# Kernel tuning notes

Hardware: AMD Instinct MI355X
Metric: run time of the kernel (lower is better)

Reference implementation:

```python
import jax, jax.numpy as jnp
import numpy as np

B, C, E, K = 16, 256, 9216, 4096  # meshes, channels, max input edges, target edges (out_channel)


def setup_inputs() -> dict:
    key = jax.random.key(0)
    k1, k2 = jax.random.split(key)
    x = jax.random.normal(k1, (B, C, E), dtype=jnp.float32)
    # ragged per-mesh edge counts, all >= K so pooling target is reachable
    edges_count = E - jax.random.randint(k2, (B,), 0, 512)
    return {"x": x, "edges_count": edges_count.astype(jnp.int64), "out_channel": K}


def reference(x, edges_count, out_channel):
    # Per-mesh edge saliency: squared sum over channels (torch.sum(x**2, dim=0)).
    score = jnp.sum(x * x, axis=1)  # [B, E]
    # Mask padded (invalid) edges beyond each mesh's edges_count so they are never kept.
    valid = jnp.arange(score.shape[-1]) < edges_count[:, None]
    score = jnp.where(valid, score, -jnp.inf)
    # Greedy collapse removes the lowest-score edges until out_channel edges remain:
    # keep the out_channel highest-score edges (descending sort + mask in the original).
    _, keep_idx = jax.lax.top_k(score, out_channel)  # [B, K]
    # Preserve original edge ordering of the surviving edges (mask-based rebuild).
    keep_idx = jnp.sort(keep_idx, axis=-1)
    # Gather surviving edge features -> [B, C, K]; matches view(B, -1, out_target).
    out = jnp.take_along_axis(x, keep_idx[:, None, :], axis=2)
    return out
```

## Files before the change

kernel.cpp:

```cpp
#include <hip/hip_runtime.h>
#include <hip/hip_bf16.h>

#define B_DIM 16
#define C_DIM 256
#define E_DIM 9216
#define K_DIM 4096
#define SEL_T 512
#define EPT   (E_DIM / SEL_T)

typedef float v4f __attribute__((ext_vector_type(4)));

__global__ __launch_bounds__(256) void score_kernel(
    const float* __restrict__ x, const void* __restrict__ ecp,
    unsigned* __restrict__ keys) {
  __shared__ double part[3][64];

  const int lane = threadIdx.x & 63;
  const int w = threadIdx.x >> 6;
  const int blk = blockIdx.x;
  const int b = blk / (E_DIM / 64);
  const int e = (blk % (E_DIM / 64)) * 64 + lane;

  const float* col =
      x + (size_t)b * C_DIM * E_DIM + (size_t)(w * 64) * E_DIM + e;

  double a0 = 0.0, a1 = 0.0;
#pragma unroll 8
  for (int c = 0; c < 64; c += 2) {
    float v0 = col[(size_t)(c + 0) * E_DIM];
    float v1 = col[(size_t)(c + 1) * E_DIM];
    a0 += (double)v0 * v0;
    a1 += (double)v1 * v1;
  }
  double s = a0 + a1;

  if (w) part[w - 1][lane] = s;
  __syncthreads();

  if (w == 0) {
    s += part[0][lane] + (part[1][lane] + part[2][lane]);

    const int* p32 = (const int*)ecp;
    long long cnt =
        (p32[1] == 0) ? ((const long long*)ecp)[b] : (long long)p32[b];

    float f = (float)s;
    keys[(size_t)b * E_DIM + (blk % (E_DIM / 64)) * 64 + lane] =
        (e < cnt) ? (__float_as_uint(f) | 0x80000000u) : 0u;
  }
}

__device__ __forceinline__ void block_scan(int val, int tid, int* wsum,
                                           int* excl, int* total) {
  int lane = tid & 63;
  int wid = tid >> 6;
  int v = val;
#pragma unroll
  for (int i = 1; i < 64; i <<= 1) {
    int t = __shfl_up(v, i, 64);
    if (lane >= i) v += t;
  }
  if (lane == 63) wsum[wid] = v;
  __syncthreads();
  int base = 0, tot = 0;
#pragma unroll
  for (int w = 0; w < SEL_T / 64; w++) {
    int s = wsum[w];
    if (w < wid) base += s;
    tot += s;
  }
  *excl = base + v - val;
  *total = tot;
  __syncthreads();
}

__global__ __launch_bounds__(SEL_T) void select_kernel(
    const unsigned* __restrict__ keys, int* __restrict__ keep) {
  __shared__ unsigned lkeys[E_DIM];
  __shared__ int hist[256];
  __shared__ int wsum[SEL_T / 64];
  __shared__ unsigned sh_prefix;
  __shared__ int sh_remK;

  const int b = blockIdx.x;
  const int tid = threadIdx.x;
  const int lane = tid & 63;

  {
    const uint2* gk = (const uint2*)(keys + (size_t)b * E_DIM);
    uint2* lk2 = (uint2*)lkeys;
    for (int i = tid; i < E_DIM / 2; i += SEL_T) lk2[i] = gk[i];
  }
  __syncthreads();

  unsigned kreg[EPT];
  const int base_e = tid * EPT;
#pragma unroll
  for (int j = 0; j < EPT; j++) kreg[j] = lkeys[base_e + j];

  unsigned prefix = 0;
  int remK = K_DIM;
#pragma unroll
  for (int pass = 3; pass >= 0; pass--) {
    const int shift = pass * 8;
    if (tid < 256) hist[tid] = 0;
    __syncthreads();

#pragma unroll
    for (int j = 0; j < EPT; j++) {
      unsigned key = kreg[j];
      bool cand = (pass == 3) || ((key >> (shift + 8)) == prefix);
      unsigned byte = (key >> shift) & 255u;
      unsigned long long m = __ballot(cand);
#pragma unroll
      for (int bit = 0; bit < 8; bit++) {
        unsigned long long bb = __ballot((byte >> bit) & 1u);
        m &= ((byte >> bit) & 1u) ? bb : ~bb;
      }
      if (cand) {
        int leader = __ffsll((unsigned long long)m) - 1;
        if (lane == leader) atomicAdd(&hist[byte], (int)__popcll(m));
      }
    }
    __syncthreads();

    int h = 0;
    if (tid < 256) h = hist[255 - tid];
    int excl, tot;
    block_scan(h, tid, wsum, &excl, &tot);
    if (tid < 256) {
      int s_incl = excl + h;
      if (s_incl >= remK && (s_incl - h) < remK) {
        sh_prefix = (prefix << 8) | (unsigned)(255 - tid);
        sh_remK = remK - (s_incl - h);
      }
    }
    __syncthreads();
    prefix = sh_prefix;
    remK = sh_remK;
  }

  const unsigned T = prefix;
  const int need_eq = remK;

  int gt_cnt = 0, eq_cnt = 0;
#pragma unroll
  for (int j = 0; j < EPT; j++) {
    gt_cnt += (kreg[j] > T);
    eq_cnt += (kreg[j] == T);
  }
  int excl, tot;
  block_scan((gt_cnt << 16) | eq_cnt, tid, wsum, &excl, &tot);
  int gt_b = excl >> 16;
  int eq_b = excl & 0xFFFF;

  int* kout = keep + b * K_DIM;
#pragma unroll
  for (int j = 0; j < EPT; j++) {
    unsigned key = kreg[j];
    if (key > T) {
      int pos = gt_b + (eq_b < need_eq ? eq_b : need_eq);
      kout[pos] = base_e + j;
      gt_b++;
    } else if (key == T) {
      if (eq_b < need_eq) kout[gt_b + eq_b] = base_e + j;
      eq_b++;
    }
  }
}

__global__ __launch_bounds__(256) void gather_kernel(
    const float* __restrict__ x, const int* __restrict__ keep,
    float* __restrict__ out) {
  int tid = blockIdx.x * blockDim.x + threadIdx.x;
  const int KQ = K_DIM / 4;
  int q = tid & (KQ - 1);
  int bc = tid >> 10;
  int b = bc >> 8;

  int4 idx4 = ((const int4*)(keep + b * K_DIM))[q];
  const float* row = x + (size_t)bc * E_DIM;
  v4f o;
  o.x = row[idx4.x];
  o.y = row[idx4.y];
  o.z = row[idx4.z];
  o.w = row[idx4.w];
  __builtin_nontemporal_store(o, (v4f*)out + tid);
}

extern "C" void kernel_launch(void* const* d_in, const int* in_sizes, int n_in,
                              void* d_out, int out_size, void* d_ws,
                              size_t ws_size, hipStream_t stream) {
  const float* x = (const float*)d_in[0];
  const void* ec = d_in[1];
  float* out = (float*)d_out;

  unsigned* keys = (unsigned*)d_ws;
  int* keep = (int*)(keys + (size_t)B_DIM * E_DIM);

  score_kernel<<<(B_DIM * E_DIM) / 64, 256, 0, stream>>>(x, ec, keys);
  select_kernel<<<B_DIM, SEL_T, 0, stream>>>(keys, keep);
  gather_kernel<<<(B_DIM * C_DIM * (K_DIM / 4)) / 256, 256, 0, stream>>>(
      x, keep, out);
}
```

Measured before the change: 279.3 us.

## Build 15-bit score histogram in score kernel to shortcut radix select passes

The score kernel now atomically accumulates a per-mesh 32768-bin global histogram over the top 16 bits of each key. The select kernel scans that histogram to find the threshold's upper 16 bits directly, compacts the candidate low halves into shared memory, and resolves the remaining two bytes with small histograms over only those candidates. This replaces the four full ballot-based radix passes over all keys. In exchange it adds a memset, global atomics in the score kernel and a 2 MB histogram read in select.

New measurement: 278.3 us. Within noise of the previous version (-0.3%).

```diff
diff --git a/kernel.cpp b/kernel.cpp
--- a/kernel.cpp
+++ b/kernel.cpp
@@ -7,12 +7,13 @@
 #define K_DIM 4096
 #define SEL_T 512
 #define EPT   (E_DIM / SEL_T)
+#define HBINS 32768
 
 typedef float v4f __attribute__((ext_vector_type(4)));
 
 __global__ __launch_bounds__(256) void score_kernel(
     const float* __restrict__ x, const void* __restrict__ ecp,
-    unsigned* __restrict__ keys) {
+    unsigned* __restrict__ keys, unsigned* __restrict__ hist) {
   __shared__ double part[3][64];
 
   const int lane = threadIdx.x & 63;
@@ -45,8 +46,10 @@
         (p32[1] == 0) ? ((const long long*)ecp)[b] : (long long)p32[b];
 
     float f = (float)s;
-    keys[(size_t)b * E_DIM + (blk % (E_DIM / 64)) * 64 + lane] =
-        (e < cnt) ? (__float_as_uint(f) | 0x80000000u) : 0u;
+    unsigned kk = (e < cnt) ? (__float_as_uint(f) | 0x80000000u) : 0u;
+    keys[(size_t)b * E_DIM + (blk % (E_DIM / 64)) * 64 + lane] = kk;
+    if (kk)
+      atomicAdd(&hist[(unsigned)b * HBINS + ((kk >> 16) & 0x7FFFu)], 1u);
   }
 }
 
@@ -75,16 +78,43 @@
 }
 
 __global__ __launch_bounds__(SEL_T) void select_kernel(
-    const unsigned* __restrict__ keys, int* __restrict__ keep) {
+    const unsigned* __restrict__ keys, const unsigned* __restrict__ hist,
+    int* __restrict__ keep) {
   __shared__ unsigned lkeys[E_DIM];
-  __shared__ int hist[256];
+  __shared__ unsigned short clist[E_DIM];
+  __shared__ int hist256[256];
   __shared__ int wsum[SEL_T / 64];
-  __shared__ unsigned sh_prefix;
-  __shared__ int sh_remK;
+  __shared__ int sh_a, sh_b;
 
   const int b = blockIdx.x;
   const int tid = threadIdx.x;
-  const int lane = tid & 63;
+
+  const unsigned* h = hist + (size_t)b * HBINS;
+  const int chunk = (SEL_T - 1) - tid;
+  const unsigned* hc = h + chunk * (HBINS / SEL_T);
+  int local = 0;
+#pragma unroll
+  for (int i = 0; i < (HBINS / SEL_T) / 4; i++) {
+    uint4 v = ((const uint4*)hc)[i];
+    local += (int)(v.x + v.y + v.z + v.w);
+  }
+  int excl, tot;
+  block_scan(local, tid, wsum, &excl, &tot);
+  if (excl < K_DIM && excl + local >= K_DIM) {
+    int run = excl;
+    for (int j = (HBINS / SEL_T) - 1; j >= 0; j--) {
+      int c = (int)hc[j];
+      if (run + c >= K_DIM) {
+        sh_a = chunk * (HBINS / SEL_T) + j;
+        sh_b = K_DIM - run;
+        break;
+      }
+      run += c;
+    }
+  }
+  __syncthreads();
+  const unsigned T16 = 0x8000u | (unsigned)sh_a;
+  int need = sh_b;
 
   {
     const uint2* gk = (const uint2*)(keys + (size_t)b * E_DIM);
@@ -98,50 +128,56 @@
 #pragma unroll
   for (int j = 0; j < EPT; j++) kreg[j] = lkeys[base_e + j];
 
-  unsigned prefix = 0;
-  int remK = K_DIM;
-#pragma unroll
-  for (int pass = 3; pass >= 0; pass--) {
-    const int shift = pass * 8;
-    if (tid < 256) hist[tid] = 0;
-    __syncthreads();
-
-#pragma unroll
-    for (int j = 0; j < EPT; j++) {
-      unsigned key = kreg[j];
-      bool cand = (pass == 3) || ((key >> (shift + 8)) == prefix);
-      unsigned byte = (key >> shift) & 255u;
-      unsigned long long m = __ballot(cand);
-#pragma unroll
-      for (int bit = 0; bit < 8; bit++) {
-        unsigned long long bb = __ballot((byte >> bit) & 1u);
-        m &= ((byte >> bit) & 1u) ? bb : ~bb;
-      }
-      if (cand) {
-        int leader = __ffsll((unsigned long long)m) - 1;
-        if (lane == leader) atomicAdd(&hist[byte], (int)__popcll(m));
-      }
-    }
-    __syncthreads();
-
-    int h = 0;
-    if (tid < 256) h = hist[255 - tid];
-    int excl, tot;
-    block_scan(h, tid, wsum, &excl, &tot);
-    if (tid < 256) {
-      int s_incl = excl + h;
-      if (s_incl >= remK && (s_incl - h) < remK) {
-        sh_prefix = (prefix << 8) | (unsigned)(255 - tid);
-        sh_remK = remK - (s_incl - h);
-      }
-    }
-    __syncthreads();
-    prefix = sh_prefix;
-    remK = sh_remK;
-  }
-
-  const unsigned T = prefix;
-  const int need_eq = remK;
+  int ccnt = 0;
+#pragma unroll
+  for (int j = 0; j < EPT; j++) ccnt += ((kreg[j] >> 16) == T16);
+  int ncand;
+  block_scan(ccnt, tid, wsum, &excl, &ncand);
+  {
+    int off = excl;
+#pragma unroll
+    for (int j = 0; j < EPT; j++)
+      if ((kreg[j] >> 16) == T16)
+        clist[off++] = (unsigned short)(kreg[j] & 0xFFFFu);
+  }
+  __syncthreads();
+
+  if (tid < 256) hist256[tid] = 0;
+  __syncthreads();
+  for (int i = tid; i < ncand; i += SEL_T)
+    atomicAdd(&hist256[clist[i] >> 8], 1);
+  __syncthreads();
+  int hh = (tid < 256) ? hist256[255 - tid] : 0;
+  block_scan(hh, tid, wsum, &excl, &tot);
+  if (tid < 256) {
+    int s_incl = excl + hh;
+    if (s_incl >= need && (s_incl - hh) < need) {
+      sh_a = 255 - tid;
+      sh_b = need - (s_incl - hh);
+    }
+  }
+  __syncthreads();
+  const int b1 = sh_a;
+  need = sh_b;
+
+  if (tid < 256) hist256[tid] = 0;
+  __syncthreads();
+  for (int i = tid; i < ncand; i += SEL_T)
+    if ((int)(clist[i] >> 8) == b1) atomicAdd(&hist256[clist[i] & 255u], 1);
+  __syncthreads();
+  hh = (tid < 256) ? hist256[255 - tid] : 0;
+  block_scan(hh, tid, wsum, &excl, &tot);
+  if (tid < 256) {
+    int s_incl = excl + hh;
+    if (s_incl >= need && (s_incl - hh) < need) {
+      sh_a = 255 - tid;
+      sh_b = need - (s_incl - hh);
+    }
+  }
+  __syncthreads();
+
+  const unsigned T = (T16 << 16) | ((unsigned)b1 << 8) | (unsigned)sh_a;
+  const int need_eq = sh_b;
 
   int gt_cnt = 0, eq_cnt = 0;
 #pragma unroll
@@ -149,7 +185,6 @@
     gt_cnt += (kreg[j] > T);
     eq_cnt += (kreg[j] == T);
   }
-  int excl, tot;
   block_scan((gt_cnt << 16) | eq_cnt, tid, wsum, &excl, &tot);
   int gt_b = excl >> 16;
   int eq_b = excl & 0xFFFF;
@@ -197,9 +232,11 @@
 
   unsigned* keys = (unsigned*)d_ws;
   int* keep = (int*)(keys + (size_t)B_DIM * E_DIM);
-
-  score_kernel<<<(B_DIM * E_DIM) / 64, 256, 0, stream>>>(x, ec, keys);
-  select_kernel<<<B_DIM, SEL_T, 0, stream>>>(keys, keep);
+  unsigned* hist = (unsigned*)(keep + (size_t)B_DIM * K_DIM);
+
+  hipMemsetAsync(hist, 0, (size_t)B_DIM * HBINS * sizeof(unsigned), stream);
+  score_kernel<<<(B_DIM * E_DIM) / 64, 256, 0, stream>>>(x, ec, keys, hist);
+  select_kernel<<<B_DIM, SEL_T, 0, stream>>>(keys, hist, keep);
   gather_kernel<<<(B_DIM * C_DIM * (K_DIM / 4)) / 256, 256, 0, stream>>>(
       x, keep, out);
 }
```
